# Kernel optimization log

Measured on AMD Instinct MI355X. Metric: run time of the kernel, lower is better.

The kernel has to match this reference:

```python
import jax, jax.numpy as jnp
import numpy as np

BETA = 0.25

def setup_inputs() -> dict:
    key = jax.random.key(0)
    k1, k2 = jax.random.split(key)
    z = jax.random.normal(k1, (32, 1024, 256), dtype=jnp.float32)
    codebook = jax.random.uniform(k2, (256, 8192), dtype=jnp.float32)  # (code_dim, num_codes)
    return {"z": z, "codebook": codebook}

def reference(z, codebook):
    code_dim = codebook.shape[0]
    z_flat = z.reshape(-1, code_dim)                                   # [N, D]
    # squared-distance matrix: ||z||^2 - 2 z@C + ||c||^2  -> [N, K]
    d = (jnp.sum(z_flat ** 2, axis=1, keepdims=True)
         - 2.0 * jnp.dot(z_flat, codebook)
         + jnp.sum(codebook ** 2, axis=0, keepdims=True))
    indices = jnp.argmin(d, axis=1)                                    # [N]
    z_q = codebook.T[indices].reshape(z.shape)                         # gather codes
    commitment_loss = BETA * jnp.mean((jax.lax.stop_gradient(z_q) - z) ** 2)
    codebook_loss = jnp.mean((z_q - jax.lax.stop_gradient(z)) ** 2)
    z_q_ste = z + jax.lax.stop_gradient(z_q - z)                       # straight-through
    loss = commitment_loss + codebook_loss
    return z_q_ste, indices.reshape(z.shape[:-1]), loss
```

## Files before the change

### kernel.cpp

```cpp
#include <hip/hip_runtime.h>
#include <hip/hip_bf16.h>
#include <stdint.h>


#define DEVINL __device__ __forceinline__

typedef int   intx4 __attribute__((ext_vector_type(4)));

#define NROWS   32768
#define DIMS    256
#define NCODES  8192
#define KMIN    ((int)0x80000000)

DEVINL int q8(float v, float s) {
  int q = __float2int_rn(v * s);
  return min(127, max(-127, q));
}
DEVINL unsigned pk4(float4 v, float s) {
  int a = q8(v.x, s), b = q8(v.y, s), c = q8(v.z, s), d = q8(v.w, s);
  return (unsigned)(a & 255) | ((unsigned)(b & 255) << 8) |
         ((unsigned)(c & 255) << 16) | ((unsigned)(d & 255) << 24);
}
DEVINL void gload_lds16(const void* g, void* lds) {
  __builtin_amdgcn_global_load_lds(
      (const __attribute__((address_space(1))) uint32_t*)(uintptr_t)g,
      (__attribute__((address_space(3))) uint32_t*)(uint32_t)(uintptr_t)lds,
      16, 0, 0);
}

__global__ void k_nrm(const float* __restrict__ cb, int* __restrict__ nrm) {
  __shared__ int p[256];
  int j = blockIdx.x * 32 + (threadIdx.x & 31);
  int seg = threadIdx.x >> 5;
  int s = 0;
  for (int i = 0; i < 32; ++i) {
    int q = q8(cb[(size_t)(seg * 32 + i) * NCODES + j], 127.0f);
    s += q * q;
  }
  p[threadIdx.x] = s;
  __syncthreads();
  if (threadIdx.x < 32) {
    int t = 0;
    for (int k = 0; k < 8; ++k) t += p[k * 32 + threadIdx.x];
    nrm[j] = (int)rintf((25.0f / 254.0f) * (float)t);
  }
}

__global__ void k_transpose(const float* __restrict__ cb, float* __restrict__ cbTf) {
  __shared__ float t[64][65];
  int j0 = blockIdx.x * 64, d0 = blockIdx.y * 64;
  int tx = threadIdx.x & 63, ty = threadIdx.x >> 6;
  #pragma unroll
  for (int i = 0; i < 16; ++i) {
    int dl = i * 4 + ty;
    t[dl][tx] = cb[(size_t)(d0 + dl) * NCODES + j0 + tx];
  }
  __syncthreads();
  #pragma unroll
  for (int i = 0; i < 16; ++i) {
    int jl = i * 4 + ty;
    cbTf[(size_t)(j0 + jl) * DIMS + d0 + tx] = t[tx][jl];
  }
}

__global__ void k_image(const float* __restrict__ cbTf, uint4* __restrict__ img) {
  int g = blockIdx.x * 256 + threadIdx.x;
  int step = g >> 11;
  int r = g & 2047;
  int wc = r >> 9, cf = (r >> 6) & 7, lgr = (r >> 4) & 3, l15 = r & 15;
  int tile = step >> 2, chunk = step & 3;
  int j = tile * 512 + wc * 128 + cf * 16 + l15;
  int d = chunk * 64 + lgr * 16;
  const float4* s4 = (const float4*)(cbTf + (size_t)j * DIMS + d);
  uint4 o;
  o.x = pk4(s4[0], 127.0f); o.y = pk4(s4[1], 127.0f);
  o.z = pk4(s4[2], 127.0f); o.w = pk4(s4[3], 127.0f);
  img[g] = o;
}

__global__ __launch_bounds__(256, 2)
void k_scan(const float* __restrict__ z, const int* __restrict__ nrm,
            const uint4* __restrict__ img, int2* __restrict__ cand) {
  __shared__ char smem[81920];
  char* const zb = smem;
  char* const bb = smem + 16384;

  const int t = threadIdx.x;
  const int lane = t & 63;
  const int wave = t >> 6;
  const int l15 = lane & 15;
  const int lgr = lane >> 4;
  const int brow = blockIdx.x * 64;

  #pragma unroll
  for (int i = 0; i < 4; ++i) {
    int g = t + i * 256;
    int row = g >> 4, kb = g & 15;
    const float4* src = (const float4*)(z + (size_t)(brow + row) * DIMS + kb * 16);
    uint4 o;
    o.x = pk4(src[0], 25.0f); o.y = pk4(src[1], 25.0f);
    o.z = pk4(src[2], 25.0f); o.w = pk4(src[3], 25.0f);
    int addr = row * 256 + ((kb * 16) ^ ((row & 15) << 4));
    *(uint4*)(zb + addr) = o;
  }
  {
    const uint4* gsrc = img + wave * 64 + lane;
    #pragma unroll
    for (int i = 0; i < 8; ++i)
      gload_lds16(gsrc + i * 256, bb + (i * 256 + wave * 64) * 16);
  }

  int k1[16], k2[16];
  #pragma unroll
  for (int i = 0; i < 16; ++i) { k1[i] = KMIN; k2[i] = KMIN; }

  __syncthreads();

  intx4 acc[4][8];

  #pragma unroll 1
  for (int s = 0; s < 64; ++s) {
    const int tile = s >> 2, chunk = s & 3;

    if (s > 0) {
      asm volatile("s_waitcnt vmcnt(0)" ::: "memory");
      __builtin_amdgcn_s_barrier();
    }
    if (s < 63) {
      const uint4* gsrc = img + (size_t)(s + 1) * 2048 + wave * 64 + lane;
      char* dst = bb + ((s + 1) & 1) * 32768;
      #pragma unroll
      for (int i = 0; i < 8; ++i)
        gload_lds16(gsrc + i * 256, dst + (i * 256 + wave * 64) * 16);
    }

    const char* cbuf = bb + (s & 1) * 32768;

    if (chunk == 0) {
      #pragma unroll
      for (int cf = 0; cf < 8; ++cf) {
        int h = -nrm[tile * 512 + wave * 128 + cf * 16 + l15];
        #pragma unroll
        for (int rf = 0; rf < 4; ++rf) acc[rf][cf] = intx4{h, h, h, h};
      }
    }

    intx4 a[4], b[8];
    #pragma unroll
    for (int rf = 0; rf < 4; ++rf) {
      int m = rf * 16 + l15;
      int by = (chunk * 64 + lgr * 16) ^ (l15 << 4);
      a[rf] = *(const intx4*)(zb + m * 256 + by);
    }
    #pragma unroll
    for (int cf = 0; cf < 8; ++cf)
      b[cf] = *(const intx4*)(cbuf + (wave * 512 + cf * 64 + lane) * 16);

    #pragma unroll
    for (int rf = 0; rf < 4; ++rf)
      #pragma unroll
      for (int cf = 0; cf < 8; ++cf)
        acc[rf][cf] = __builtin_amdgcn_mfma_i32_16x16x64_i8(a[rf], b[cf], acc[rf][cf], 0, 0, 0);

    if (chunk == 3) {
      const int jinvb = 8191 - (tile * 512 + wave * 128 + l15);
      #pragma unroll
      for (int rf = 0; rf < 4; ++rf)
        #pragma unroll
        for (int cf = 0; cf < 8; ++cf) {
          int jinv = jinvb - cf * 16;
          #pragma unroll
          for (int r = 0; r < 4; ++r) {
            int si = rf * 4 + r;
            int k = ((acc[rf][cf][r] >> 5) << 13) + jinv;
            int t1 = max(k1[si], k);
            int t2 = min(k1[si], k);
            k1[si] = t1;
            k2[si] = max(k2[si], t2);
          }
        }
    }
  }

  #pragma unroll
  for (int rf = 0; rf < 4; ++rf)
    #pragma unroll
    for (int r = 0; r < 4; ++r) {
      int row = brow + rf * 16 + lgr * 4 + r;
      int si = rf * 4 + r;
      cand[(size_t)row * 64 + wave * 16 + l15] = make_int2(k1[si], k2[si]);
    }
}

__global__ __launch_bounds__(512)
void k_refine(const float* __restrict__ z, const float* __restrict__ cbTf,
              const int2* __restrict__ cand, float* __restrict__ zq,
              float* __restrict__ oidx, double* __restrict__ parts) {
  __shared__ double lsum[8];
  int lane = threadIdx.x & 63, wave = threadIdx.x >> 6;
  int row = blockIdx.x * 8 + wave;

  float4 z4 = ((const float4*)(z + (size_t)row * DIMS))[lane];
  int2 kp = cand[(size_t)row * 64 + lane];
  int ka = kp.x, kb = kp.y;

  double bd = 1e300; int bj = -1; float4 bc = {0.f, 0.f, 0.f, 0.f};
  for (int s = 0; s < 5; ++s) {
    int km = max(ka, kb);
    #pragma unroll
    for (int m = 1; m < 64; m <<= 1) km = max(km, __shfl_xor(km, m, 64));
    int j = 8191 - (km & 8191);
    if (ka == km) ka = KMIN; else if (kb == km) kb = KMIN;

    float4 c4 = ((const float4*)(cbTf + (size_t)j * DIMS))[lane];
    double dx = (double)z4.x - (double)c4.x;
    double dy = (double)z4.y - (double)c4.y;
    double dzv = (double)z4.z - (double)c4.z;
    double dw = (double)z4.w - (double)c4.w;
    double d = dx * dx + dy * dy + dzv * dzv + dw * dw;
    #pragma unroll
    for (int m = 1; m < 64; m <<= 1) d += __shfl_xor(d, m, 64);

    bool bt = (d < bd) || (d == bd && j < bj);
    if (bt) { bd = d; bj = j; bc = c4; }
  }

  ((float4*)(zq + (size_t)row * DIMS))[lane] = bc;
  if (lane == 0) oidx[row] = (float)bj;

  double lx = (double)bc.x - (double)z4.x;
  double ly = (double)bc.y - (double)z4.y;
  double lz = (double)bc.z - (double)z4.z;
  double lw = (double)bc.w - (double)z4.w;
  double l = lx * lx + ly * ly + lz * lz + lw * lw;
  #pragma unroll
  for (int m = 1; m < 64; m <<= 1) l += __shfl_xor(l, m, 64);
  if (lane == 0) lsum[wave] = l;
  __syncthreads();
  if (threadIdx.x == 0) {
    double s = 0;
    for (int i = 0; i < 8; ++i) s += lsum[i];
    parts[blockIdx.x] = s;
  }
}

__global__ void k_finish(const double* __restrict__ parts, float* __restrict__ out) {
  __shared__ double s[256];
  double a = 0;
  for (int i = threadIdx.x; i < 4096; i += 256) a += parts[i];
  s[threadIdx.x] = a;
  __syncthreads();
  for (int w = 128; w; w >>= 1) {
    if (threadIdx.x < w) s[threadIdx.x] += s[threadIdx.x + w];
    __syncthreads();
  }
  if (threadIdx.x == 0) out[0] = (float)(1.25 * s[0] / 8388608.0);
}

extern "C" void kernel_launch(void* const* d_in, const int* in_sizes, int n_in,
                              void* d_out, int out_size, void* d_ws, size_t ws_size,
                              hipStream_t stream) {
  const float* zin = (const float*)d_in[0];
  const float* cb  = (const float*)d_in[1];
  float* out = (float*)d_out;

  char* w = (char*)d_ws;
  int*    nrm   = (int*)w;
  float*  cbTf  = (float*)(w + 32768);
  char*   imgb  = w + 32768 + 8388608;
  int2*   cand  = (int2*)(w + 32768 + 8388608 + 2097152);
  double* parts = (double*)(w + 32768 + 8388608 + 2097152 + 16777216);

  float* zq_out   = out;
  float* idx_out  = out + 8388608;
  float* loss_out = out + 8388608 + 32768;

  k_nrm<<<dim3(256), dim3(256), 0, stream>>>(cb, nrm);
  k_transpose<<<dim3(128, 4), dim3(256), 0, stream>>>(cb, cbTf);
  k_image<<<dim3(512), dim3(256), 0, stream>>>(cbTf, (uint4*)imgb);
  k_scan<<<dim3(512), dim3(256), 0, stream>>>(zin, nrm, (const uint4*)imgb, cand);
  k_refine<<<dim3(4096), dim3(512), 0, stream>>>(zin, cbTf, cand, zq_out, idx_out, parts);
  k_finish<<<dim3(1), dim3(256), 0, stream>>>(parts, loss_out);
}
```

Baseline: 163.8 us.

## Split scan block into 8 waves over a 2x4 row/column wave grid

The scan kernel now launches 512 threads per block instead of 256. The waves form a 2x4 grid, so each wave covers 32 rows and 128 codes instead of 64 rows and 128 codes. This halves the accumulator and top-2 register state per wave, aiming for more resident waves to hide LDS and global-load latency. The cost is that each codebook fragment is read from LDS by two waves, so per-wave MFMA reuse of B drops and LDS read traffic doubles; the LDS footprint of 80KB per block may also limit co-residency.

```diff
diff --git a/kernel.cpp b/kernel.cpp
--- a/kernel.cpp
+++ b/kernel.cpp
@@ -78,7 +78,7 @@
   img[g] = o;
 }
 
-__global__ __launch_bounds__(256, 2)
+__global__ __launch_bounds__(512, 4)
 void k_scan(const float* __restrict__ z, const int* __restrict__ nrm,
             const uint4* __restrict__ img, int2* __restrict__ cand) {
   __shared__ char smem[81920];
@@ -88,13 +88,15 @@
   const int t = threadIdx.x;
   const int lane = t & 63;
   const int wave = t >> 6;
+  const int wgr = wave >> 2;
+  const int wc  = wave & 3;
   const int l15 = lane & 15;
   const int lgr = lane >> 4;
   const int brow = blockIdx.x * 64;
 
   #pragma unroll
-  for (int i = 0; i < 4; ++i) {
-    int g = t + i * 256;
+  for (int i = 0; i < 2; ++i) {
+    int g = t + i * 512;
     int row = g >> 4, kb = g & 15;
     const float4* src = (const float4*)(z + (size_t)(brow + row) * DIMS + kb * 16);
     uint4 o;
@@ -106,17 +108,17 @@
   {
     const uint4* gsrc = img + wave * 64 + lane;
     #pragma unroll
-    for (int i = 0; i < 8; ++i)
-      gload_lds16(gsrc + i * 256, bb + (i * 256 + wave * 64) * 16);
-  }
-
-  int k1[16], k2[16];
-  #pragma unroll
-  for (int i = 0; i < 16; ++i) { k1[i] = KMIN; k2[i] = KMIN; }
-
-  __syncthreads();
-
-  intx4 acc[4][8];
+    for (int i = 0; i < 4; ++i)
+      gload_lds16(gsrc + i * 512, bb + (i * 512 + wave * 64) * 16);
+  }
+
+  int k1[8], k2[8];
+  #pragma unroll
+  for (int i = 0; i < 8; ++i) { k1[i] = KMIN; k2[i] = KMIN; }
+
+  __syncthreads();
+
+  intx4 acc[2][8];
 
   #pragma unroll 1
   for (int s = 0; s < 64; ++s) {
@@ -130,8 +132,8 @@
       const uint4* gsrc = img + (size_t)(s + 1) * 2048 + wave * 64 + lane;
       char* dst = bb + ((s + 1) & 1) * 32768;
       #pragma unroll
-      for (int i = 0; i < 8; ++i)
-        gload_lds16(gsrc + i * 256, dst + (i * 256 + wave * 64) * 16);
+      for (int i = 0; i < 4; ++i)
+        gload_lds16(gsrc + i * 512, dst + (i * 512 + wave * 64) * 16);
     }
 
     const char* cbuf = bb + (s & 1) * 32768;
@@ -139,33 +141,30 @@
     if (chunk == 0) {
       #pragma unroll
       for (int cf = 0; cf < 8; ++cf) {
-        int h = -nrm[tile * 512 + wave * 128 + cf * 16 + l15];
-        #pragma unroll
-        for (int rf = 0; rf < 4; ++rf) acc[rf][cf] = intx4{h, h, h, h};
+        int h = -nrm[tile * 512 + wc * 128 + cf * 16 + l15];
+        acc[0][cf] = intx4{h, h, h, h};
+        acc[1][cf] = intx4{h, h, h, h};
       }
     }
 
-    intx4 a[4], b[8];
-    #pragma unroll
-    for (int rf = 0; rf < 4; ++rf) {
-      int m = rf * 16 + l15;
+    intx4 a[2];
+    #pragma unroll
+    for (int rf = 0; rf < 2; ++rf) {
+      int m = wgr * 32 + rf * 16 + l15;
       int by = (chunk * 64 + lgr * 16) ^ (l15 << 4);
       a[rf] = *(const intx4*)(zb + m * 256 + by);
     }
     #pragma unroll
-    for (int cf = 0; cf < 8; ++cf)
-      b[cf] = *(const intx4*)(cbuf + (wave * 512 + cf * 64 + lane) * 16);
-
-    #pragma unroll
-    for (int rf = 0; rf < 4; ++rf)
+    for (int cf = 0; cf < 8; ++cf) {
+      intx4 b = *(const intx4*)(cbuf + (wc * 512 + cf * 64 + lane) * 16);
+      acc[0][cf] = __builtin_amdgcn_mfma_i32_16x16x64_i8(a[0], b, acc[0][cf], 0, 0, 0);
+      acc[1][cf] = __builtin_amdgcn_mfma_i32_16x16x64_i8(a[1], b, acc[1][cf], 0, 0, 0);
+    }
+
+    if (chunk == 3) {
+      const int jinvb = 8191 - (tile * 512 + wc * 128 + l15);
       #pragma unroll
-      for (int cf = 0; cf < 8; ++cf)
-        acc[rf][cf] = __builtin_amdgcn_mfma_i32_16x16x64_i8(a[rf], b[cf], acc[rf][cf], 0, 0, 0);
-
-    if (chunk == 3) {
-      const int jinvb = 8191 - (tile * 512 + wave * 128 + l15);
-      #pragma unroll
-      for (int rf = 0; rf < 4; ++rf)
+      for (int rf = 0; rf < 2; ++rf)
         #pragma unroll
         for (int cf = 0; cf < 8; ++cf) {
           int jinv = jinvb - cf * 16;
@@ -183,12 +182,12 @@
   }
 
   #pragma unroll
-  for (int rf = 0; rf < 4; ++rf)
+  for (int rf = 0; rf < 2; ++rf)
     #pragma unroll
     for (int r = 0; r < 4; ++r) {
-      int row = brow + rf * 16 + lgr * 4 + r;
+      int row = brow + wgr * 32 + rf * 16 + lgr * 4 + r;
       int si = rf * 4 + r;
-      cand[(size_t)row * 64 + wave * 16 + l15] = make_int2(k1[si], k2[si]);
+      cand[(size_t)row * 64 + wc * 16 + l15] = make_int2(k1[si], k2[si]);
     }
 }
 
@@ -278,7 +277,7 @@
   k_nrm<<<dim3(256), dim3(256), 0, stream>>>(cb, nrm);
   k_transpose<<<dim3(128, 4), dim3(256), 0, stream>>>(cb, cbTf);
   k_image<<<dim3(512), dim3(256), 0, stream>>>(cbTf, (uint4*)imgb);
-  k_scan<<<dim3(512), dim3(256), 0, stream>>>(zin, nrm, (const uint4*)imgb, cand);
+  k_scan<<<dim3(512), dim3(512), 0, stream>>>(zin, nrm, (const uint4*)imgb, cand);
   k_refine<<<dim3(4096), dim3(512), 0, stream>>>(zin, cbTf, cand, zq_out, idx_out, parts);
   k_finish<<<dim3(1), dim3(256), 0, stream>>>(parts, loss_out);
 }
```

After: 163.6 us. Within noise of the previous version (-0.1%).
